# Kernel optimization log

Hardware: AMD Instinct MI355X
Metric: run time of the kernel (lower is better)

The kernel has to match this reference:

```python
import jax, jax.numpy as jnp
import numpy as np

NFEATS = 768; NHIDS = 768; H = 8; HD = NHIDS // H
NT = 32768; NC = 32768; NS = 32768; DEG = 8; E = NT * DEG
ALPHA = 0.2  # LeakyReLU negative slope


def setup_inputs() -> dict:
    key = jax.random.key(0)
    ks = jax.random.split(key, 16)
    f32 = jnp.float32
    dst = jnp.repeat(jnp.arange(NT, dtype=jnp.int32), DEG)  # uniform in-degree mailbox
    return {
        'h': jax.random.normal(ks[0], (NT, NFEATS), f32),
        'hb_c_src': jax.random.normal(ks[1], (NC, NHIDS), f32),
        'hb_s_src': jax.random.normal(ks[2], (NS, NHIDS), f32),
        'Wg': jax.random.normal(ks[3], (H, NFEATS, HD), f32) * 0.05,
        'bg': jnp.zeros((H, HD), f32),
        'ag': jax.random.normal(ks[4], (H, 2 * HD), f32) * 0.1,
        'agb': jnp.zeros((H,), f32),
        'Wx': jax.random.normal(ks[5], (H, NHIDS, HD), f32) * 0.05,
        'bx': jnp.zeros((H, HD), f32),
        'ax': jax.random.normal(ks[6], (H, 2 * HD), f32) * 0.1,
        'axb': jnp.zeros((H,), f32),
        'Wih': jax.random.normal(ks[7], (3 * NHIDS, NHIDS), f32) * 0.02,
        'Whh': jax.random.normal(ks[8], (3 * NHIDS, NHIDS), f32) * 0.02,
        'bih': jnp.zeros((3 * NHIDS,), f32),
        'bhh': jnp.zeros((3 * NHIDS,), f32),
        'intra_src': jax.random.randint(ks[9], (E,), 0, NT, jnp.int32),
        'intra_dst': dst,
        'c_src': jax.random.randint(ks[10], (E,), 0, NC, jnp.int32),
        'c_dst': dst,
        's_src': jax.random.randint(ks[11], (E,), 0, NS, jnp.int32),
        's_dst': dst,
    }


def _attend(Wh_s, Wh_d, src, dst, a, ab, n_dst):
    """Multi-head GAT edge attention + segment softmax + weighted aggregation.
    Wh_s: [Ns,H,D] src projections, Wh_d: [Nd,H,D] dst projections.
    a([Wh_src||Wh_dst]) decomposed as a_src.Wh_src + a_dst.Wh_dst + bias."""
    D = Wh_s.shape[-1]
    e = (jnp.einsum('nhd,hd->nh', Wh_s, a[:, :D])[src]
         + jnp.einsum('nhd,hd->nh', Wh_d, a[:, D:])[dst] + ab)  # [E,H]
    e = jax.nn.leaky_relu(e, ALPHA)
    m = jax.ops.segment_max(e, dst, num_segments=n_dst)
    ex = jnp.exp(e - m[dst])
    den = jax.ops.segment_sum(ex, dst, num_segments=n_dst)
    att = ex / den[dst]  # per-dst softmax over incoming edges (DGL mailbox softmax)
    out = jax.ops.segment_sum(Wh_s[src] * att[..., None], dst, num_segments=n_dst)
    return out.reshape(n_dst, H * D)  # concat heads


def _forward(h, hb_c_src, hb_s_src, Wg, bg, ag, agb, Wx, bx, ax, axb,
             Wih, Whh, bih, bhh, intra_src, intra_dst, c_src, c_dst, s_src, s_dst):
    n = h.shape[0]
    # intra-turn GAT (x = self.gat(g, t)); dropout is identity in eval mode
    Wh = jnp.einsum('nf,hfd->nhd', h, Wg) + bg
    x = _attend(Wh, Wh, intra_src, intra_dst, ag, agb, n)
    # cross-turn inversed GAT; dst nodes' 'hb' feature is the fresh gat output x;
    # counter_bw and support_bw share the same xgat weights.
    Wx_d = jnp.einsum('nf,hfd->nhd', x, Wx) + bx
    Wc_s = jnp.einsum('nf,hfd->nhd', hb_c_src, Wx) + bx
    h_c = _attend(Wc_s, Wx_d, c_src, c_dst, ax, axb, n)
    Ws_s = jnp.einsum('nf,hfd->nhd', hb_s_src, Wx) + bx
    h_s = _attend(Ws_s, Wx_d, s_src, s_dst, ax, axb, n)
    hid = 0.5 * h_c + 0.5 * h_s
    # GRUCell(x, hid)
    gi = x @ Wih.T + bih
    gh = hid @ Whh.T + bhh
    ir, iz, inn = jnp.split(gi, 3, axis=1)
    hr, hz, hn = jnp.split(gh, 3, axis=1)
    r = jax.nn.sigmoid(ir + hr)
    z = jax.nn.sigmoid(iz + hz)
    cand = jnp.tanh(inn + r * hn)
    return (1.0 - z) * cand + z * hid


def reference(h, hb_c_src, hb_s_src, Wg, bg, ag, agb, Wx, bx, ax, axb,
              Wih, Whh, bih, bhh, intra_src, intra_dst, c_src, c_dst, s_src, s_dst):
    return _forward(h, hb_c_src, hb_s_src, Wg, bg, ag, agb, Wx, bx, ax, axb,
                    Wih, Whh, bih, bhh, intra_src, intra_dst, c_src, c_dst, s_src, s_dst)
```

## Files before the change

kernel.cpp:

```cpp
#include <hip/hip_runtime.h>
#include <hip/hip_bf16.h>
#include <math.h>

#define NT 32768
#define HD 96
#define DEG 8
#define NE (NT * DEG)
#define LRELU_ALPHA 0.2f
#define CH 8192

typedef __attribute__((ext_vector_type(8))) short bf16x8;
typedef __attribute__((ext_vector_type(8))) unsigned short u16x8;
typedef __attribute__((ext_vector_type(4))) unsigned short u16x4;
typedef __attribute__((ext_vector_type(4))) float f32x4;

__device__ __forceinline__ unsigned short f2bf(float x) {
    union { float f; unsigned u; } v; v.f = x;
    unsigned r = v.u + 0x7FFFu + ((v.u >> 16) & 1u);
    return (unsigned short)(r >> 16);
}
__device__ __forceinline__ float bf2f(unsigned short u) {
    union { unsigned u; float f; } v; v.u = ((unsigned)u) << 16; return v.f;
}

__device__ __forceinline__ void gload_lds16(const void* g, void* l) {
    __builtin_amdgcn_global_load_lds(
        (const __attribute__((address_space(1))) void*)g,
        (__attribute__((address_space(3))) void*)l, 16, 0, 0);
}


__global__ void packWT(const float* __restrict__ W, unsigned short* __restrict__ T) {
    int idx = blockIdx.x * 256 + threadIdx.x;
    if (idx >= 768 * 768) return;
    int c = idx / 768, f = idx % 768;
    T[idx] = f2bf(W[(size_t)(c / HD) * 768 * HD + (size_t)f * HD + (c % HD)]);
}

__global__ void cvt_bf8(const float* __restrict__ X, unsigned short* __restrict__ Y, int n8) {
    int i = blockIdx.x * 256 + threadIdx.x;
    if (i >= n8) return;
    float4 a = ((const float4*)X)[2 * i];
    float4 b = ((const float4*)X)[2 * i + 1];
    u16x8 p;
    p[0] = f2bf(a.x); p[1] = f2bf(a.y); p[2] = f2bf(a.z); p[3] = f2bf(a.w);
    p[4] = f2bf(b.x); p[5] = f2bf(b.y); p[6] = f2bf(b.z); p[7] = f2bf(b.w);
    ((u16x8*)Y)[i] = p;
}

__global__ __launch_bounds__(256, 4) void mgemm_bb(
    const unsigned short* __restrict__ A, const unsigned short* __restrict__ BT,
    const float* __restrict__ bias, unsigned short* __restrict__ C,
    int M, int N, int K) {
    __shared__ unsigned short Alds[2][128 * 32];
    __shared__ unsigned short Blds[2][128 * 32];
    const int tid = threadIdx.x;
    const int w = tid >> 6, l = tid & 63;
    const int wr = w >> 1, wc = w & 1;
    const int lrow = l & 15, lk = l >> 4;

    const int nx = gridDim.x;
    const int nwg = nx * gridDim.y;
    int lin = blockIdx.y * nx + blockIdx.x;
    if ((nwg & 7) == 0) lin = (lin & 7) * (nwg >> 3) + (lin >> 3);
    const int bm = lin / nx, bn = lin % nx;

    const unsigned short* asrc[2];
    const unsigned short* bsrc[2];
    #pragma unroll
    for (int q = 0; q < 2; q++) {
        int idx = q * 256 + tid;
        int r = idx >> 2, s = idx & 3;
        int kw = s ^ ((r >> 1) & 3);
        asrc[q] = A  + (size_t)(bm * 128 + r) * K + kw * 8;
        bsrc[q] = BT + (size_t)(bn * 128 + r) * K + kw * 8;
    }
    const int ldst = (w * 64) * 8;

    gload_lds16(asrc[0], &Alds[0][ldst]);
    gload_lds16(asrc[1], &Alds[0][2048 + ldst]);
    gload_lds16(bsrc[0], &Blds[0][ldst]);
    gload_lds16(bsrc[1], &Blds[0][2048 + ldst]);

    f32x4 acc[4][4] = {};
    const int nt = K >> 5;

    for (int t = 0; t < nt; ++t) {
        const int cur = t & 1;
        __syncthreads();
        if (t + 1 < nt) {
            const int k1 = (t + 1) << 5;
            gload_lds16(asrc[0] + k1, &Alds[cur ^ 1][ldst]);
            gload_lds16(asrc[1] + k1, &Alds[cur ^ 1][2048 + ldst]);
            gload_lds16(bsrc[0] + k1, &Blds[cur ^ 1][ldst]);
            gload_lds16(bsrc[1] + k1, &Blds[cur ^ 1][2048 + ldst]);
        }
        bf16x8 af[4], bfv[4];
        #pragma unroll
        for (int i = 0; i < 4; i++) {
            int r = wr * 64 + i * 16 + lrow;
            int s = lk ^ ((r >> 1) & 3);
            af[i] = *(const bf16x8*)(&Alds[cur][r * 32 + s * 8]);
        }
        #pragma unroll
        for (int j = 0; j < 4; j++) {
            int r = wc * 64 + j * 16 + lrow;
            int s = lk ^ ((r >> 1) & 3);
            bfv[j] = *(const bf16x8*)(&Blds[cur][r * 32 + s * 8]);
        }
        #pragma unroll
        for (int i = 0; i < 4; i++)
            #pragma unroll
            for (int j = 0; j < 4; j++)
                acc[i][j] = __builtin_amdgcn_mfma_f32_16x16x32_bf16(af[i], bfv[j], acc[i][j], 0, 0, 0);
    }

    const size_t crow0 = (size_t)bm * 128 + wr * 64;
    const int ccol0 = bn * 128 + wc * 64;
    #pragma unroll
    for (int j = 0; j < 4; j++) {
        int col = ccol0 + j * 16 + lrow;
        float bv = bias[col];
        #pragma unroll
        for (int i = 0; i < 4; i++) {
            size_t row = crow0 + i * 16 + lk * 4;
            #pragma unroll
            for (int e = 0; e < 4; e++)
                C[(row + e) * N + col] = f2bf(acc[i][j][e] + bv);
        }
    }
}

__global__ __launch_bounds__(256) void escore2(
    const unsigned short* __restrict__ X, const float* __restrict__ a,
    float* __restrict__ s0out, float* __restrict__ s1out) {
    __shared__ float av0[768], av1[768];
    for (int t = threadIdx.x; t < 768; t += 256) {
        int hh = t / HD, d = t % HD;
        av0[t] = a[hh * 2 * HD + d];
        av1[t] = a[hh * 2 * HD + HD + d];
    }
    __syncthreads();
    int idx = blockIdx.x * 256 + threadIdx.x;
    int row = idx >> 3, hh = idx & 7;
    const unsigned short* xp = X + (size_t)row * 768 + hh * HD;
    const float* a0 = av0 + hh * HD;
    const float* a1 = av1 + hh * HD;
    float s0 = 0.f, s1 = 0.f;
    #pragma unroll
    for (int q = 0; q < 12; q++) {
        u16x8 v = *(const u16x8*)(xp + q * 8);
        #pragma unroll
        for (int e = 0; e < 8; e++) {
            float x = bf2f(v[e]);
            s0 += x * a0[q * 8 + e];
            s1 += x * a1[q * 8 + e];
        }
    }
    s0out[idx] = s0;
    s1out[idx] = s1;
}

__global__ __launch_bounds__(256) void escore(
    const unsigned short* __restrict__ X, const float* __restrict__ a,
    int half, float* __restrict__ sc) {
    __shared__ float av[768];
    for (int t = threadIdx.x; t < 768; t += 256) {
        int hh = t / HD, d = t % HD;
        av[t] = a[hh * 2 * HD + half * HD + d];
    }
    __syncthreads();
    int idx = blockIdx.x * 256 + threadIdx.x;
    int row = idx >> 3, hh = idx & 7;
    const unsigned short* xp = X + (size_t)row * 768 + hh * HD;
    const float* ap = av + hh * HD;
    float s = 0.f;
    #pragma unroll
    for (int q = 0; q < 12; q++) {
        u16x8 v = *(const u16x8*)(xp + q * 8);
        #pragma unroll
        for (int e = 0; e < 8; e++) s += bf2f(v[e]) * ap[q * 8 + e];
    }
    sc[idx] = s;
}

__global__ __launch_bounds__(256) void attend_agg(
    const unsigned short* __restrict__ Whs, const float* __restrict__ es,
    const float* __restrict__ ed, const float* __restrict__ ab,
    const int* __restrict__ src, const int* __restrict__ dst,
    unsigned short* __restrict__ out) {
    const int wv = threadIdx.x >> 6, l = threadIdx.x & 63;
    const int seg = blockIdx.x * 4 + wv;
    const int hh = l >> 3, j = l & 7;
    int sj = src[seg * 8 + j];
    int dnode = dst[seg * 8];
    float e = es[(size_t)sj * 8 + hh] + ed[(size_t)dnode * 8 + hh] + ab[hh];
    e = e > 0.f ? e : LRELU_ALPHA * e;
    float m = e;
    #pragma unroll
    for (int o = 1; o < 8; o <<= 1) m = fmaxf(m, __shfl_xor(m, o, 64));
    float ex = expf(e - m);
    float s = ex;
    #pragma unroll
    for (int o = 1; o < 8; o <<= 1) s += __shfl_xor(s, o, 64);
    float att = ex / s;

    #pragma unroll
    for (int u = 0; u < 3; u++) {
        int c = 4 * l + 256 * u;
        int h = c / HD;
        float acc0 = 0.f, acc1 = 0.f, acc2 = 0.f, acc3 = 0.f;
        #pragma unroll
        for (int j2 = 0; j2 < 8; j2++) {
            float a = __shfl(att, h * 8 + j2, 64);
            int sid = __shfl(sj, j2, 64);
            u16x4 v = *(const u16x4*)(Whs + (size_t)sid * 768 + c);
            acc0 += a * bf2f(v[0]); acc1 += a * bf2f(v[1]);
            acc2 += a * bf2f(v[2]); acc3 += a * bf2f(v[3]);
        }
        u16x4 r;
        r[0] = f2bf(acc0); r[1] = f2bf(acc1); r[2] = f2bf(acc2); r[3] = f2bf(acc3);
        *(u16x4*)(out + (size_t)dnode * 768 + c) = r;
    }
}

__global__ __launch_bounds__(256) void attend2(
    const unsigned short* __restrict__ Wc, const unsigned short* __restrict__ Ws,
    const float* __restrict__ esC, const float* __restrict__ esS,
    const float* __restrict__ ed, const float* __restrict__ ab,
    const int* __restrict__ csrc, const int* __restrict__ ssrc,
    const int* __restrict__ dst, unsigned short* __restrict__ outH) {
    const int wv = threadIdx.x >> 6, l = threadIdx.x & 63;
    const int seg = blockIdx.x * 4 + wv;
    const int hh = l >> 3, j = l & 7;
    int cj = csrc[seg * 8 + j];
    int sj = ssrc[seg * 8 + j];
    int dnode = dst[seg * 8];
    float edv = ed[(size_t)dnode * 8 + hh] + ab[hh];

    float eC = esC[(size_t)cj * 8 + hh] + edv;
    eC = eC > 0.f ? eC : LRELU_ALPHA * eC;
    float mC = eC;
    #pragma unroll
    for (int o = 1; o < 8; o <<= 1) mC = fmaxf(mC, __shfl_xor(mC, o, 64));
    float exC = expf(eC - mC);
    float sC = exC;
    #pragma unroll
    for (int o = 1; o < 8; o <<= 1) sC += __shfl_xor(sC, o, 64);
    float attC = exC / sC;

    float eS = esS[(size_t)sj * 8 + hh] + edv;
    eS = eS > 0.f ? eS : LRELU_ALPHA * eS;
    float mS = eS;
    #pragma unroll
    for (int o = 1; o < 8; o <<= 1) mS = fmaxf(mS, __shfl_xor(mS, o, 64));
    float exS = expf(eS - mS);
    float sS = exS;
    #pragma unroll
    for (int o = 1; o < 8; o <<= 1) sS += __shfl_xor(sS, o, 64);
    float attS = exS / sS;

    #pragma unroll
    for (int u = 0; u < 3; u++) {
        int c = 4 * l + 256 * u;
        int h = c / HD;
        float acc0 = 0.f, acc1 = 0.f, acc2 = 0.f, acc3 = 0.f;
        #pragma unroll
        for (int j2 = 0; j2 < 8; j2++) {
            float a = __shfl(attC, h * 8 + j2, 64);
            int sid = __shfl(cj, j2, 64);
            u16x4 v = *(const u16x4*)(Wc + (size_t)sid * 768 + c);
            acc0 += a * bf2f(v[0]); acc1 += a * bf2f(v[1]);
            acc2 += a * bf2f(v[2]); acc3 += a * bf2f(v[3]);
        }
        #pragma unroll
        for (int j2 = 0; j2 < 8; j2++) {
            float a = __shfl(attS, h * 8 + j2, 64);
            int sid = __shfl(sj, j2, 64);
            u16x4 v = *(const u16x4*)(Ws + (size_t)sid * 768 + c);
            acc0 += a * bf2f(v[0]); acc1 += a * bf2f(v[1]);
            acc2 += a * bf2f(v[2]); acc3 += a * bf2f(v[3]);
        }
        u16x4 r;
        r[0] = f2bf(0.5f * acc0); r[1] = f2bf(0.5f * acc1);
        r[2] = f2bf(0.5f * acc2); r[3] = f2bf(0.5f * acc3);
        *(u16x4*)(outH + (size_t)dnode * 768 + c) = r;
    }
}

__global__ __launch_bounds__(256) void gru_elem(
    const unsigned short* __restrict__ gi, const unsigned short* __restrict__ gh,
    const unsigned short* __restrict__ hid, float* __restrict__ out) {
    int idx = blockIdx.x * 256 + threadIdx.x;
    int nrow = idx / 96, c8 = (idx % 96) * 8;
    const unsigned short* gip = gi + (size_t)nrow * 2304 + c8;
    const unsigned short* ghp = gh + (size_t)nrow * 2304 + c8;
    u16x8 vir = *(const u16x8*)(gip);
    u16x8 viz = *(const u16x8*)(gip + 768);
    u16x8 vin = *(const u16x8*)(gip + 1536);
    u16x8 vhr = *(const u16x8*)(ghp);
    u16x8 vhz = *(const u16x8*)(ghp + 768);
    u16x8 vhn = *(const u16x8*)(ghp + 1536);
    u16x8 vh  = *(const u16x8*)(hid + (size_t)nrow * 768 + c8);
    float res[8];
    #pragma unroll
    for (int e = 0; e < 8; e++) {
        float r = 1.f / (1.f + expf(-(bf2f(vir[e]) + bf2f(vhr[e]))));
        float z = 1.f / (1.f + expf(-(bf2f(viz[e]) + bf2f(vhz[e]))));
        float cand = tanhf(bf2f(vin[e]) + r * bf2f(vhn[e]));
        res[e] = (1.f - z) * cand + z * bf2f(vh[e]);
    }
    float* op = out + (size_t)nrow * 768 + c8;
    *(float4*)(op)     = make_float4(res[0], res[1], res[2], res[3]);
    *(float4*)(op + 4) = make_float4(res[4], res[5], res[6], res[7]);
}

extern "C" void kernel_launch(void* const* d_in, const int* in_sizes, int n_in,
                              void* d_out, int out_size, void* d_ws, size_t ws_size,
                              hipStream_t stream) {
    const float* h    = (const float*)d_in[0];
    const float* hbc  = (const float*)d_in[1];
    const float* hbs  = (const float*)d_in[2];
    const float* Wg   = (const float*)d_in[3];
    const float* bg   = (const float*)d_in[4];
    const float* ag   = (const float*)d_in[5];
    const float* agb  = (const float*)d_in[6];
    const float* Wx   = (const float*)d_in[7];
    const float* bx   = (const float*)d_in[8];
    const float* ax   = (const float*)d_in[9];
    const float* axb  = (const float*)d_in[10];
    const float* Wih  = (const float*)d_in[11];
    const float* Whh  = (const float*)d_in[12];
    const float* bih  = (const float*)d_in[13];
    const float* bhh  = (const float*)d_in[14];
    const int* i_src  = (const int*)d_in[15];
    const int* i_dst  = (const int*)d_in[16];
    const int* c_src  = (const int*)d_in[17];
    const int* c_dst  = (const int*)d_in[18];
    const int* s_src  = (const int*)d_in[19];
    const int* s_dst  = (const int*)d_in[20];
    float* out = (float*)d_out;

    const size_t SZ = (size_t)NT * 768;
    unsigned short* Xb  = (unsigned short*)d_ws;
    unsigned short* Hdb = Xb + SZ;
    unsigned short* GIb = Hdb + SZ;
    unsigned short* GHb = GIb + (size_t)CH * 2304;
    unsigned short* AB  = GIb;
    unsigned short* W2gT = GHb + (size_t)CH * 2304;
    unsigned short* W2xT = W2gT + 768 * 768;
    unsigned short* WihB = W2xT + 768 * 768;
    unsigned short* WhhB = WihB + 2304 * 768;
    float* ES  = (float*)(WhhB + 2304 * 768);
    float* ED  = ES + NE;
    float* ESI = ED + NE;
    float* EDI = ESI + NE;
    unsigned short* P2b = (unsigned short*)(EDI + NE);
    unsigned short* Pb = (unsigned short*)d_out;

    dim3 blk(256);
    packWT<<<(768 * 768 + 255) / 256, blk, 0, stream>>>(Wg, W2gT);
    packWT<<<(768 * 768 + 255) / 256, blk, 0, stream>>>(Wx, W2xT);
    cvt_bf8<<<(2304 * 768 / 8 + 255) / 256, blk, 0, stream>>>(Wih, WihB, 2304 * 768 / 8);
    cvt_bf8<<<(2304 * 768 / 8 + 255) / 256, blk, 0, stream>>>(Whh, WhhB, 2304 * 768 / 8);

    dim3 g768(6, NT / 128);
    const int n8 = (int)(SZ / 8);
    const int cvtg = (n8 + 255) / 256;

    cvt_bf8<<<cvtg, blk, 0, stream>>>(h, AB, n8);
    mgemm_bb<<<g768, blk, 0, stream>>>(AB, W2gT, bg, Pb, NT, 768, 768);
    escore2<<<NE / 256, blk, 0, stream>>>(Pb, ag, ESI, EDI);
    attend_agg<<<NT / 4, blk, 0, stream>>>(Pb, ESI, EDI, agb, i_src, i_dst, Xb);
    mgemm_bb<<<g768, blk, 0, stream>>>(Xb, W2xT, bx, Pb, NT, 768, 768);
    escore<<<NE / 256, blk, 0, stream>>>(Pb, ax, 1, ED);
    cvt_bf8<<<cvtg, blk, 0, stream>>>(hbc, AB, n8);
    mgemm_bb<<<g768, blk, 0, stream>>>(AB, W2xT, bx, Pb, NT, 768, 768);
    escore<<<NE / 256, blk, 0, stream>>>(Pb, ax, 0, ES);
    cvt_bf8<<<cvtg, blk, 0, stream>>>(hbs, AB, n8);
    mgemm_bb<<<g768, blk, 0, stream>>>(AB, W2xT, bx, P2b, NT, 768, 768);
    escore<<<NE / 256, blk, 0, stream>>>(P2b, ax, 0, ESI);
    attend2<<<NT / 4, blk, 0, stream>>>(Pb, P2b, ES, ESI, ED, axb, c_src, s_src, c_dst, Hdb);

    dim3 gch(2304 / 128, CH / 128);
    for (int c0 = 0; c0 < NT; c0 += CH) {
        mgemm_bb<<<gch, blk, 0, stream>>>(Xb  + (size_t)c0 * 768, WihB, bih, GIb, CH, 2304, 768);
        mgemm_bb<<<gch, blk, 0, stream>>>(Hdb + (size_t)c0 * 768, WhhB, bhh, GHb, CH, 2304, 768);
        gru_elem<<<(CH * 96) / 256, blk, 0, stream>>>(GIb, GHb, Hdb + (size_t)c0 * 768, out + (size_t)c0 * 768);
    }
}
```

Baseline: 1.010 ms.

## Fold Wx·ax into per-head vectors, batch src GEMMs, enlarge GRU chunks

The destination-side attention score for the cross-turn GAT is now computed directly from the intra-GAT output. Wx is pre-contracted with ax and bx into a small 8x768 vector set, so the full 32768x768x768 projection GEMM of x is dropped. The counter and support source projections are merged into a single GEMM over 2*NT rows, with one escore launch over both. The GRU chunk size is doubled to cut launch count. This changes rounding, because the score now uses bf16 x against fp32 folded weights, and it enlarges workspace and output scratch use, since Pcat spans two NT×768 bf16 buffers inside d_out.

```diff
diff --git a/kernel.cpp b/kernel.cpp
--- a/kernel.cpp
+++ b/kernel.cpp
@@ -7,7 +7,7 @@
 #define DEG 8
 #define NE (NT * DEG)
 #define LRELU_ALPHA 0.2f
-#define CH 8192
+#define CH 16384
 
 typedef __attribute__((ext_vector_type(8))) short bf16x8;
 typedef __attribute__((ext_vector_type(8))) unsigned short u16x8;
@@ -46,6 +46,27 @@
     p[0] = f2bf(a.x); p[1] = f2bf(a.y); p[2] = f2bf(a.z); p[3] = f2bf(a.w);
     p[4] = f2bf(b.x); p[5] = f2bf(b.y); p[6] = f2bf(b.z); p[7] = f2bf(b.w);
     ((u16x8*)Y)[i] = p;
+}
+
+__global__ void packWV(const float* __restrict__ Wx, const float* __restrict__ ax,
+                       const float* __restrict__ bx,
+                       float* __restrict__ wv, float* __restrict__ cd) {
+    int idx = blockIdx.x * 256 + threadIdx.x;
+    if (idx < 8 * 768) {
+        int h = idx / 768, f = idx % 768;
+        const float* wp = Wx + (size_t)h * 768 * HD + (size_t)f * HD;
+        const float* ap = ax + h * 2 * HD + HD;
+        float s = 0.f;
+        for (int d = 0; d < HD; d++) s += wp[d] * ap[d];
+        wv[idx] = s;
+    }
+    if (idx < 8) {
+        const float* bp = bx + idx * HD;
+        const float* ap = ax + idx * 2 * HD + HD;
+        float s = 0.f;
+        for (int d = 0; d < HD; d++) s += bp[d] * ap[d];
+        cd[idx] = s;
+    }
 }
 
 __global__ __launch_bounds__(256, 4) void mgemm_bb(
@@ -182,6 +203,38 @@
         for (int e = 0; e < 8; e++) s += bf2f(v[e]) * ap[q * 8 + e];
     }
     sc[idx] = s;
+}
+
+__global__ __launch_bounds__(256) void escore_fold(
+    const unsigned short* __restrict__ X, const float* __restrict__ wv,
+    const float* __restrict__ cd, float* __restrict__ ed) {
+    __shared__ float wvs[8][8][97];
+    __shared__ float cds[8];
+    for (int i = threadIdx.x; i < 8 * 8 * 96; i += 256) {
+        int j = i / (8 * 96); int r = i % (8 * 96); int h = r / 96; int t = r % 96;
+        wvs[j][h][t] = wv[h * 768 + j * 96 + t];
+    }
+    if (threadIdx.x < 8) cds[threadIdx.x] = cd[threadIdx.x];
+    __syncthreads();
+    int idx = blockIdx.x * 256 + threadIdx.x;
+    int n = idx >> 3, j = idx & 7;
+    const unsigned short* xp = X + (size_t)n * 768 + j * 96;
+    float p[8] = {};
+    #pragma unroll
+    for (int q = 0; q < 12; q++) {
+        u16x8 v = *(const u16x8*)(xp + q * 8);
+        #pragma unroll
+        for (int e = 0; e < 8; e++) {
+            float x = bf2f(v[e]);
+            #pragma unroll
+            for (int h = 0; h < 8; h++) p[h] += x * wvs[j][h][q * 8 + e];
+        }
+    }
+    #pragma unroll
+    for (int o = 1; o < 8; o <<= 1)
+        #pragma unroll
+        for (int h = 0; h < 8; h++) p[h] += __shfl_xor(p[h], o, 64);
+    ed[(size_t)n * 8 + j] = p[j] + cds[j];
 }
 
 __global__ __launch_bounds__(256) void attend_agg(
@@ -342,46 +395,47 @@
     float* out = (float*)d_out;
 
     const size_t SZ = (size_t)NT * 768;
-    unsigned short* Xb  = (unsigned short*)d_ws;
-    unsigned short* Hdb = Xb + SZ;
-    unsigned short* GIb = Hdb + SZ;
-    unsigned short* GHb = GIb + (size_t)CH * 2304;
-    unsigned short* AB  = GIb;
+    unsigned short* Xb   = (unsigned short*)d_ws;
+    unsigned short* Hdb  = Xb + SZ;
+    unsigned short* GIb  = Hdb + SZ;
+    unsigned short* GHb  = GIb + (size_t)CH * 2304;
+    unsigned short* ABc  = GIb;
+    unsigned short* ABs  = GIb + SZ;
     unsigned short* W2gT = GHb + (size_t)CH * 2304;
     unsigned short* W2xT = W2gT + 768 * 768;
     unsigned short* WihB = W2xT + 768 * 768;
     unsigned short* WhhB = WihB + 2304 * 768;
-    float* ES  = (float*)(WhhB + 2304 * 768);
-    float* ED  = ES + NE;
-    float* ESI = ED + NE;
-    float* EDI = ESI + NE;
-    unsigned short* P2b = (unsigned short*)(EDI + NE);
-    unsigned short* Pb = (unsigned short*)d_out;
+    float* EScat = (float*)(WhhB + 2304 * 768);
+    float* ED    = EScat + 2 * NE;
+    float* ESI   = ED + NE;
+    float* EDI   = ESI + NE;
+    float* WV    = EDI + NE;
+    float* CD    = WV + 8 * 768;
+    unsigned short* Pcat = (unsigned short*)d_out;
 
     dim3 blk(256);
     packWT<<<(768 * 768 + 255) / 256, blk, 0, stream>>>(Wg, W2gT);
     packWT<<<(768 * 768 + 255) / 256, blk, 0, stream>>>(Wx, W2xT);
     cvt_bf8<<<(2304 * 768 / 8 + 255) / 256, blk, 0, stream>>>(Wih, WihB, 2304 * 768 / 8);
     cvt_bf8<<<(2304 * 768 / 8 + 255) / 256, blk, 0, stream>>>(Whh, WhhB, 2304 * 768 / 8);
+    packWV<<<(8 * 768 + 255) / 256, blk, 0, stream>>>(Wx, ax, bx, WV, CD);
 
     dim3 g768(6, NT / 128);
+    dim3 gcat(6, 2 * NT / 128);
     const int n8 = (int)(SZ / 8);
     const int cvtg = (n8 + 255) / 256;
 
-    cvt_bf8<<<cvtg, blk, 0, stream>>>(h, AB, n8);
-    mgemm_bb<<<g768, blk, 0, stream>>>(AB, W2gT, bg, Pb, NT, 768, 768);
-    escore2<<<NE / 256, blk, 0, stream>>>(Pb, ag, ESI, EDI);
-    attend_agg<<<NT / 4, blk, 0, stream>>>(Pb, ESI, EDI, agb, i_src, i_dst, Xb);
-    mgemm_bb<<<g768, blk, 0, stream>>>(Xb, W2xT, bx, Pb, NT, 768, 768);
-    escore<<<NE / 256, blk, 0, stream>>>(Pb, ax, 1, ED);
-    cvt_bf8<<<cvtg, blk, 0, stream>>>(hbc, AB, n8);
-    mgemm_bb<<<g768, blk, 0, stream>>>(AB, W2xT, bx, Pb, NT, 768, 768);
-    escore<<<NE / 256, blk, 0, stream>>>(Pb, ax, 0, ES);
-    cvt_bf8<<<cvtg, blk, 0, stream>>>(hbs, AB, n8);
-    mgemm_bb<<<g768, blk, 0, stream>>>(AB, W2xT, bx, P2b, NT, 768, 768);
-    escore<<<NE / 256, blk, 0, stream>>>(P2b, ax, 0, ESI);
-    attend2<<<NT / 4, blk, 0, stream>>>(Pb, P2b, ES, ESI, ED, axb, c_src, s_src, c_dst, Hdb);
-
+    cvt_bf8<<<cvtg, blk, 0, stream>>>(h, ABc, n8);
+    mgemm_bb<<<g768, blk, 0, stream>>>(ABc, W2gT, bg, Pcat, NT, 768, 768);
+    escore2<<<NE / 256, blk, 0, stream>>>(Pcat, ag, ESI, EDI);
+    attend_agg<<<NT / 4, blk, 0, stream>>>(Pcat, ESI, EDI, agb, i_src, i_dst, Xb);
+    escore_fold<<<NE / 256, blk, 0, stream>>>(Xb, WV, CD, ED);
+    cvt_bf8<<<cvtg, blk, 0, stream>>>(hbc, ABc, n8);
+    cvt_bf8<<<cvtg, blk, 0, stream>>>(hbs, ABs, n8);
+    mgemm_bb<<<gcat, blk, 0, stream>>>(ABc, W2xT, bx, Pcat, 2 * NT, 768, 768);
+    escore<<<2 * NE / 256, blk, 0, stream>>>(Pcat, ax, 0, EScat);
+    attend2<<<NT / 4, blk, 0, stream>>>(Pcat, Pcat + SZ, EScat, EScat + NE, ED, axb,
+                                        c_src, s_src, c_dst, Hdb);
     dim3 gch(2304 / 128, CH / 128);
     for (int c0 = 0; c0 < NT; c0 += CH) {
         mgemm_bb<<<gch, blk, 0, stream>>>(Xb  + (size_t)c0 * 768, WihB, bih, GIb, CH, 2304, 768);
```

Measured after the change: 927.1 us. -8.2%, faster.
